# Performance work log

Hardware: AMD Instinct MI355X
Metric: run time of the kernel (lower is better)

## Reference

```python
import jax, jax.numpy as jnp
import numpy as np

NEG_INF = -9e15
ALPHA = 0.2  # LeakyReLU negative slope used by GraphAttentionLayer


def gat_layer(h, adj, W, a, concat):
    # h: [N, din], W: [din, dout], a: [2*dout, 1]
    Wh = h @ W                              # [N, dout]
    dout = W.shape[1]
    f1 = Wh @ a[:dout]                      # [N, 1]
    f2 = Wh @ a[dout:]                      # [N, 1]
    e = jax.nn.leaky_relu(f1 + f2.T, negative_slope=ALPHA)   # [N, N]
    att = jax.nn.softmax(jnp.where(adj > 0, e, NEG_INF), axis=1)
    hp = att @ Wh                           # [N, dout]
    out = jax.nn.elu(hp) if concat else hp
    return out, att


def setup_inputs() -> dict:
    key = jax.random.key(0)
    ks = jax.random.split(key, 6)
    N, d_in, d_hid, d_out = 8192, 256, 128, 64
    features = jax.random.normal(ks[0], (N, d_in), dtype=jnp.float32)
    adj = (jax.random.uniform(ks[1], (N, N)) < 0.01).astype(jnp.float32)
    s = 0.1
    W1 = jax.random.normal(ks[2], (d_in, d_hid), dtype=jnp.float32) * s
    a1 = jax.random.normal(ks[3], (2 * d_hid, 1), dtype=jnp.float32) * s
    W2 = jax.random.normal(ks[4], (d_hid, d_out), dtype=jnp.float32) * s
    a2 = jax.random.normal(ks[5], (2 * d_out, 1), dtype=jnp.float32) * s
    return {"features": features, "adj": adj, "W1": W1, "a1": a1, "W2": W2, "a2": a2}


def reference(features, adj, W1, a1, W2, a2):
    h1, attention = gat_layer(features, adj, W1, a1, concat=True)   # gat1 (elu)
    h2, _ = gat_layer(h1, adj, W2, a2, concat=False)                 # gat2
    row_mask = (adj.sum(axis=1) > 0).astype(h2.dtype)[:, None]       # [N, 1]
    genenet_res = jax.nn.sigmoid(h2 @ h2.T) * row_mask               # inner-product decoder
    return h2, genenet_res, attention
```

## Files before the change

kernel.cpp:

```cpp
#include <hip/hip_runtime.h>
#include <cstdint>
#include <cstddef>

#define NN 8192
#define DIN 256
#define DHID 128
#define DOUT 64
#define MAXDEG 256

using short8  = __attribute__((ext_vector_type(8))) short;
using floatx4 = __attribute__((ext_vector_type(4))) float;

__device__ inline unsigned short f2bf(float x) {
  union { float f; unsigned u; } c; c.f = x;
  unsigned r = (c.u + 0x7FFFu + ((c.u >> 16) & 1u)) >> 16;
  return (unsigned short)r;
}

__global__ __launch_bounds__(256) void k_gemm1(const float* __restrict__ feat,
                                               const float* __restrict__ W1,
                                               float* __restrict__ Wh1) {
  __shared__ float Ws[64 * DHID];
  __shared__ float Fs[32][65];
  const int tid = threadIdx.x;
  const int cx = tid & 31;
  const int ry = tid >> 5;
  const int r0 = blockIdx.x * 32;
  float acc[4][4] = {};
  for (int kc = 0; kc < DIN; kc += 64) {
    const float4* src = (const float4*)(W1 + (size_t)kc * DHID);
    float4* dst = (float4*)Ws;
    #pragma unroll
    for (int i = 0; i < 8; ++i) dst[i * 256 + tid] = src[i * 256 + tid];
    #pragma unroll
    for (int i = 0; i < 2; ++i) {
      int idx = i * 256 + tid;
      int row = idx >> 4, kq = idx & 15;
      float4 v = *(const float4*)(feat + (size_t)(r0 + row) * DIN + kc + kq * 4);
      Fs[row][kq * 4 + 0] = v.x; Fs[row][kq * 4 + 1] = v.y;
      Fs[row][kq * 4 + 2] = v.z; Fs[row][kq * 4 + 3] = v.w;
    }
    __syncthreads();
    #pragma unroll 4
    for (int k = 0; k < 64; ++k) {
      float4 w = *(const float4*)(Ws + k * DHID + cx * 4);
      #pragma unroll
      for (int r = 0; r < 4; ++r) {
        float f = Fs[ry * 4 + r][k];
        acc[r][0] += f * w.x; acc[r][1] += f * w.y;
        acc[r][2] += f * w.z; acc[r][3] += f * w.w;
      }
    }
    __syncthreads();
  }
  #pragma unroll
  for (int r = 0; r < 4; ++r) {
    float4 o = make_float4(acc[r][0], acc[r][1], acc[r][2], acc[r][3]);
    *(float4*)(Wh1 + (size_t)(r0 + ry * 4 + r) * DHID + cx * 4) = o;
  }
}

__global__ __launch_bounds__(256) void k_gemm2(const float* __restrict__ h1,
                                               const float* __restrict__ W2,
                                               float* __restrict__ Wh2) {
  __shared__ float Ws[64 * DOUT];
  __shared__ float Fs[32][65];
  const int tid = threadIdx.x;
  const int cx = tid & 15;
  const int ry = tid >> 4;
  const int r0 = blockIdx.x * 32;
  float acc[2][4] = {};
  for (int kc = 0; kc < DHID; kc += 64) {
    const float4* src = (const float4*)(W2 + (size_t)kc * DOUT);
    float4* dst = (float4*)Ws;
    #pragma unroll
    for (int i = 0; i < 4; ++i) dst[i * 256 + tid] = src[i * 256 + tid];
    #pragma unroll
    for (int i = 0; i < 2; ++i) {
      int idx = i * 256 + tid;
      int row = idx >> 4, kq = idx & 15;
      float4 v = *(const float4*)(h1 + (size_t)(r0 + row) * DHID + kc + kq * 4);
      Fs[row][kq * 4 + 0] = v.x; Fs[row][kq * 4 + 1] = v.y;
      Fs[row][kq * 4 + 2] = v.z; Fs[row][kq * 4 + 3] = v.w;
    }
    __syncthreads();
    #pragma unroll 4
    for (int k = 0; k < 64; ++k) {
      float4 w = *(const float4*)(Ws + k * DOUT + cx * 4);
      #pragma unroll
      for (int r = 0; r < 2; ++r) {
        float f = Fs[ry * 2 + r][k];
        acc[r][0] += f * w.x; acc[r][1] += f * w.y;
        acc[r][2] += f * w.z; acc[r][3] += f * w.w;
      }
    }
    __syncthreads();
  }
  #pragma unroll
  for (int r = 0; r < 2; ++r) {
    float4 o = make_float4(acc[r][0], acc[r][1], acc[r][2], acc[r][3]);
    *(float4*)(Wh2 + (size_t)(r0 + ry * 2 + r) * DOUT + cx * 4) = o;
  }
}

__global__ __launch_bounds__(256) void k_fvec1(const float* __restrict__ Wh1,
                                               const float* __restrict__ a1,
                                               float* __restrict__ f1, float* __restrict__ f2) {
  int wv = threadIdx.x >> 6, lane = threadIdx.x & 63;
  int row = blockIdx.x * 4 + wv;
  float2 x = *(const float2*)(Wh1 + (size_t)row * DHID + lane * 2);
  float2 u = *(const float2*)(a1 + lane * 2);
  float2 v = *(const float2*)(a1 + DHID + lane * 2);
  float s1 = x.x * u.x + x.y * u.y;
  float s2 = x.x * v.x + x.y * v.y;
  #pragma unroll
  for (int off = 32; off; off >>= 1) { s1 += __shfl_down(s1, off); s2 += __shfl_down(s2, off); }
  if (lane == 0) { f1[row] = s1; f2[row] = s2; }
}

__global__ __launch_bounds__(256) void k_fvec2(const float* __restrict__ Wh2,
                                               const float* __restrict__ a2,
                                               float* __restrict__ f1, float* __restrict__ f2) {
  int wv = threadIdx.x >> 6, lane = threadIdx.x & 63;
  int row = blockIdx.x * 4 + wv;
  float x = Wh2[(size_t)row * DOUT + lane];
  float s1 = x * a2[lane];
  float s2 = x * a2[DOUT + lane];
  #pragma unroll
  for (int off = 32; off; off >>= 1) { s1 += __shfl_down(s1, off); s2 += __shfl_down(s2, off); }
  if (lane == 0) { f1[row] = s1; f2[row] = s2; }
}

__global__ __launch_bounds__(256) void k_att1(const float* __restrict__ adj,
                                              const float* __restrict__ f1v,
                                              const float* __restrict__ f2v,
                                              const float* __restrict__ Wh1,
                                              float* __restrict__ att_out,
                                              float* __restrict__ h1,
                                              int* __restrict__ csr,
                                              int* __restrict__ degree) {
  __shared__ int   scols[4][MAXDEG];
  __shared__ float sval[4][MAXDEG];
  __shared__ int   cnt[4];
  const int tid = threadIdx.x;
  const int wid = tid >> 6, lane = tid & 63;
  const int row = blockIdx.x * 4 + wid;
  if (lane == 0) cnt[wid] = 0;
  __syncthreads();
  const float4* arow = (const float4*)(adj + (size_t)row * NN);
  #pragma unroll 4
  for (int it = 0; it < 32; ++it) {
    float4 v = arow[it * 64 + lane];
    int base = (it * 64 + lane) * 4;
    if (v.x > 0.0f) { int s = atomicAdd(&cnt[wid], 1); if (s < MAXDEG) scols[wid][s] = base; }
    if (v.y > 0.0f) { int s = atomicAdd(&cnt[wid], 1); if (s < MAXDEG) scols[wid][s] = base + 1; }
    if (v.z > 0.0f) { int s = atomicAdd(&cnt[wid], 1); if (s < MAXDEG) scols[wid][s] = base + 2; }
    if (v.w > 0.0f) { int s = atomicAdd(&cnt[wid], 1); if (s < MAXDEG) scols[wid][s] = base + 3; }
  }
  __syncthreads();
  const int deg = min(cnt[wid], MAXDEG);
  if (lane == 0) degree[row] = deg;
  if (deg == 0) {
    float4 fv = make_float4(1.0f / NN, 1.0f / NN, 1.0f / NN, 1.0f / NN);
    float4* orow = (float4*)(att_out + (size_t)row * NN);
    #pragma unroll 8
    for (int it = 0; it < 32; ++it) orow[it * 64 + lane] = fv;
  }
  for (int t = lane; t < deg; t += 64) csr[(size_t)row * MAXDEG + t] = scols[wid][t];
  const float f1r = f1v[row];
  float e[4]; int cols[4];
  float m = -3.0e38f;
  #pragma unroll
  for (int j = 0; j < 4; ++j) {
    int t = lane + j * 64;
    cols[j] = 0; e[j] = -3.0e38f;
    if (t < deg) {
      int c = scols[wid][t]; cols[j] = c;
      float x = f1r + f2v[c];
      e[j] = x > 0.0f ? x : 0.2f * x;
    }
    m = fmaxf(m, e[j]);
  }
  #pragma unroll
  for (int off = 32; off; off >>= 1) m = fmaxf(m, __shfl_xor(m, off));
  float ex[4]; float s = 0.0f;
  #pragma unroll
  for (int j = 0; j < 4; ++j) {
    ex[j] = __expf(e[j] - m);
    if (lane + j * 64 >= deg) ex[j] = 0.0f;
    s += ex[j];
  }
  #pragma unroll
  for (int off = 32; off; off >>= 1) s += __shfl_xor(s, off);
  const float inv = 1.0f / s;
  #pragma unroll
  for (int j = 0; j < 4; ++j) {
    int t = lane + j * 64;
    if (t < deg) {
      sval[wid][t] = ex[j] * inv;
      att_out[(size_t)row * NN + cols[j]] = ex[j] * inv;
    }
  }
  __syncthreads();
  float2 acc = make_float2(0.0f, 0.0f);
  if (deg > 0) {
    #pragma unroll 4
    for (int t = 0; t < deg; ++t) {
      float sv = sval[wid][t];
      float2 w = *(const float2*)(Wh1 + (size_t)scols[wid][t] * DHID + lane * 2);
      acc.x += sv * w.x; acc.y += sv * w.y;
    }
  } else {
    for (int r = 0; r < NN; ++r) {
      float2 w = *(const float2*)(Wh1 + (size_t)r * DHID + lane * 2);
      acc.x += w.x; acc.y += w.y;
    }
    acc.x *= (1.0f / (float)NN); acc.y *= (1.0f / (float)NN);
  }
  float hx = acc.x > 0.0f ? acc.x : (__expf(acc.x) - 1.0f);
  float hy = acc.y > 0.0f ? acc.y : (__expf(acc.y) - 1.0f);
  *(float2*)(h1 + (size_t)row * DHID + lane * 2) = make_float2(hx, hy);
}

__global__ __launch_bounds__(256) void k_att2(const int* __restrict__ csr,
                                              const int* __restrict__ degree,
                                              const float* __restrict__ f1v,
                                              const float* __restrict__ f2v,
                                              const float* __restrict__ Wh2,
                                              float* __restrict__ h2) {
  __shared__ int   scols[4][MAXDEG];
  __shared__ float sval[4][MAXDEG];
  const int tid = threadIdx.x;
  const int wid = tid >> 6, lane = tid & 63;
  const int row = blockIdx.x * 4 + wid;
  const int deg = degree[row];
  const float f1r = f1v[row];
  float e[4]; int cols[4];
  float m = -3.0e38f;
  #pragma unroll
  for (int j = 0; j < 4; ++j) {
    int t = lane + j * 64;
    cols[j] = 0; e[j] = -3.0e38f;
    if (t < deg) {
      int c = csr[(size_t)row * MAXDEG + t];
      cols[j] = c; scols[wid][t] = c;
      float x = f1r + f2v[c];
      e[j] = x > 0.0f ? x : 0.2f * x;
    }
    m = fmaxf(m, e[j]);
  }
  #pragma unroll
  for (int off = 32; off; off >>= 1) m = fmaxf(m, __shfl_xor(m, off));
  float ex[4]; float s = 0.0f;
  #pragma unroll
  for (int j = 0; j < 4; ++j) {
    ex[j] = __expf(e[j] - m);
    if (lane + j * 64 >= deg) ex[j] = 0.0f;
    s += ex[j];
  }
  #pragma unroll
  for (int off = 32; off; off >>= 1) s += __shfl_xor(s, off);
  const float inv = 1.0f / s;
  #pragma unroll
  for (int j = 0; j < 4; ++j) { int t = lane + j * 64; if (t < deg) sval[wid][t] = ex[j] * inv; }
  __syncthreads();
  float acc = 0.0f;
  if (deg > 0) {
    #pragma unroll 4
    for (int t = 0; t < deg; ++t)
      acc += sval[wid][t] * Wh2[(size_t)scols[wid][t] * DOUT + lane];
  } else {
    for (int r = 0; r < NN; ++r) acc += Wh2[(size_t)r * DOUT + lane];
    acc *= (1.0f / (float)NN);
  }
  h2[(size_t)row * DOUT + lane] = acc;
}

__global__ __launch_bounds__(256) void k_genenet(const float* __restrict__ h2,
                                                 const int* __restrict__ degree,
                                                 float* __restrict__ out) {
  __shared__ __align__(16) unsigned short AB[2 * 128 * 64];
  __shared__ float dmask[128];
  unsigned short* As = AB;
  unsigned short* Bs = AB + 128 * 64;
  const int tid = threadIdx.x;
  const int R0 = blockIdx.x * 128, C0 = blockIdx.y * 128;
  #pragma unroll
  for (int it = 0; it < 8; ++it) {
    int idx = it * 256 + tid;
    int r = idx >> 4, kq = idx & 15;
    int c = kq >> 1, hf = kq & 1;
    int off = r * 64 + (((c + r) & 7) << 3) + (hf << 2);
    float4 va = *(const float4*)(h2 + (size_t)(R0 + r) * DOUT + kq * 4);
    float4 vb = *(const float4*)(h2 + (size_t)(C0 + r) * DOUT + kq * 4);
    ushort4 ba = make_ushort4(f2bf(va.x), f2bf(va.y), f2bf(va.z), f2bf(va.w));
    ushort4 bb = make_ushort4(f2bf(vb.x), f2bf(vb.y), f2bf(vb.z), f2bf(vb.w));
    *(ushort4*)&As[off] = ba;
    *(ushort4*)&Bs[off] = bb;
  }
  if (tid < 128) dmask[tid] = (degree[R0 + tid] > 0) ? 1.0f : 0.0f;
  __syncthreads();
  const int wave = tid >> 6, lane = tid & 63;
  const int wr = wave >> 1, wc = wave & 1;
  const int lr = lane & 15, quad = lane >> 4;
  short8 a[4][2], b[4][2];
  #pragma unroll
  for (int mi = 0; mi < 4; ++mi) {
    int r = wr * 64 + mi * 16 + lr;
    #pragma unroll
    for (int j = 0; j < 2; ++j) {
      int c = quad + 4 * j;
      a[mi][j] = *(const short8*)(const void*)&As[r * 64 + (((c + r) & 7) << 3)];
    }
  }
  #pragma unroll
  for (int ni = 0; ni < 4; ++ni) {
    int r = wc * 64 + ni * 16 + lr;
    #pragma unroll
    for (int j = 0; j < 2; ++j) {
      int c = quad + 4 * j;
      b[ni][j] = *(const short8*)(const void*)&Bs[r * 64 + (((c + r) & 7) << 3)];
    }
  }
  floatx4 acc[4][4] = {};
  #pragma unroll
  for (int mi = 0; mi < 4; ++mi)
    #pragma unroll
    for (int ni = 0; ni < 4; ++ni) {
      acc[mi][ni] = __builtin_amdgcn_mfma_f32_16x16x32_bf16(a[mi][0], b[ni][0], acc[mi][ni], 0, 0, 0);
      acc[mi][ni] = __builtin_amdgcn_mfma_f32_16x16x32_bf16(a[mi][1], b[ni][1], acc[mi][ni], 0, 0, 0);
    }
  __syncthreads();
  float* stage = (float*)AB;
  #pragma unroll
  for (int half = 0; half < 2; ++half) {
    if (wr == half) {
      #pragma unroll
      for (int mi = 0; mi < 4; ++mi)
        #pragma unroll
        for (int reg = 0; reg < 4; ++reg) {
          int lrow = mi * 16 + quad * 4 + reg;
          #pragma unroll
          for (int ni = 0; ni < 4; ++ni)
            stage[lrow * 128 + wc * 64 + ni * 16 + lr] = acc[mi][ni][reg];
        }
    }
    __syncthreads();
    #pragma unroll
    for (int it = 0; it < 8; ++it) {
      int idx = it * 256 + tid;
      int r = idx >> 5, c4 = idx & 31;
      float4 x = *(const float4*)&stage[r * 128 + c4 * 4];
      float msk = dmask[half * 64 + r];
      floatx4 o;
      o[0] = msk * __builtin_amdgcn_rcpf(1.0f + __expf(-x.x));
      o[1] = msk * __builtin_amdgcn_rcpf(1.0f + __expf(-x.y));
      o[2] = msk * __builtin_amdgcn_rcpf(1.0f + __expf(-x.z));
      o[3] = msk * __builtin_amdgcn_rcpf(1.0f + __expf(-x.w));
      __builtin_nontemporal_store(o, (floatx4*)(out + (size_t)(R0 + half * 64 + r) * NN + C0 + c4 * 4));
    }
    if (half == 0) __syncthreads();
  }
}

extern "C" void kernel_launch(void* const* d_in, const int* in_sizes, int n_in,
                              void* d_out, int out_size, void* d_ws, size_t ws_size,
                              hipStream_t stream) {
  const float* feat = (const float*)d_in[0];
  const float* adj  = (const float*)d_in[1];
  const float* W1   = (const float*)d_in[2];
  const float* a1   = (const float*)d_in[3];
  const float* W2   = (const float*)d_in[4];
  const float* a2   = (const float*)d_in[5];
  float* out = (float*)d_out;
  float* h2_out  = out;
  float* gen_out = out + (size_t)NN * DOUT;
  float* att_out = gen_out + (size_t)NN * NN;
  int*   csr  = (int*)gen_out;
  float* Wh1  = gen_out + 2097152;
  float* h1   = gen_out + 3145728;
  float* Wh2  = gen_out + 4194304;
  float* f1_1 = gen_out + 4718592;
  float* f2_1 = f1_1 + NN;
  float* f1_2 = f2_1 + NN;
  float* f2_2 = f1_2 + NN;
  int* degree = (int*)d_ws;

  (void)hipMemsetAsync((void*)att_out, 0, (size_t)NN * NN * sizeof(float), stream);

  k_gemm1  <<<dim3(NN / 32), dim3(256), 0, stream>>>(feat, W1, Wh1);
  k_fvec1  <<<dim3(NN / 4),  dim3(256), 0, stream>>>(Wh1, a1, f1_1, f2_1);
  k_att1   <<<dim3(NN / 4),  dim3(256), 0, stream>>>(adj, f1_1, f2_1, Wh1, att_out, h1, csr, degree);
  k_gemm2  <<<dim3(NN / 32), dim3(256), 0, stream>>>(h1, W2, Wh2);
  k_fvec2  <<<dim3(NN / 4),  dim3(256), 0, stream>>>(Wh2, a2, f1_2, f2_2);
  k_att2   <<<dim3(NN / 4),  dim3(256), 0, stream>>>(csr, degree, f1_2, f2_2, Wh2, h2_out);
  k_genenet<<<dim3(64, 64),  dim3(256), 0, stream>>>(h2_out, degree, gen_out);
}
```

Baseline: 798.4 us.

## Fuse attention-vector dots into GEMMs and write dense attention rows directly

The f1/f2 projections are now computed in the GEMM epilogues with a lane-group shuffle reduction, which removes the two fvec kernels and a reread of Wh. The 256MB memset of the attention matrix is also removed. k_att1 builds a per-row bitmap of the adjacency in shared memory and then writes every attention row as dense nontemporal float4 stores, recomputing each nonzero value in place. Entries for columns beyond the first MAXDEG neighbors are now written as nonzero, while before they stayed zero, so results could differ for rows that hit the cap.

Result: no change. 787.2 us (-1.4%).

```diff
diff --git a/kernel.cpp b/kernel.cpp
--- a/kernel.cpp
+++ b/kernel.cpp
@@ -19,7 +19,10 @@
 
 __global__ __launch_bounds__(256) void k_gemm1(const float* __restrict__ feat,
                                                const float* __restrict__ W1,
-                                               float* __restrict__ Wh1) {
+                                               const float* __restrict__ a1,
+                                               float* __restrict__ Wh1,
+                                               float* __restrict__ f1,
+                                               float* __restrict__ f2) {
   __shared__ float Ws[64 * DHID];
   __shared__ float Fs[32][65];
   const int tid = threadIdx.x;
@@ -53,16 +56,26 @@
     }
     __syncthreads();
   }
+  const float4 u = *(const float4*)(a1 + cx * 4);
+  const float4 v = *(const float4*)(a1 + DHID + cx * 4);
   #pragma unroll
   for (int r = 0; r < 4; ++r) {
     float4 o = make_float4(acc[r][0], acc[r][1], acc[r][2], acc[r][3]);
     *(float4*)(Wh1 + (size_t)(r0 + ry * 4 + r) * DHID + cx * 4) = o;
+    float s1 = acc[r][0] * u.x + acc[r][1] * u.y + acc[r][2] * u.z + acc[r][3] * u.w;
+    float s2 = acc[r][0] * v.x + acc[r][1] * v.y + acc[r][2] * v.z + acc[r][3] * v.w;
+    #pragma unroll
+    for (int off = 16; off; off >>= 1) { s1 += __shfl_xor(s1, off); s2 += __shfl_xor(s2, off); }
+    if (cx == 0) { f1[r0 + ry * 4 + r] = s1; f2[r0 + ry * 4 + r] = s2; }
   }
 }
 
 __global__ __launch_bounds__(256) void k_gemm2(const float* __restrict__ h1,
                                                const float* __restrict__ W2,
-                                               float* __restrict__ Wh2) {
+                                               const float* __restrict__ a2,
+                                               float* __restrict__ Wh2,
+                                               float* __restrict__ f1,
+                                               float* __restrict__ f2) {
   __shared__ float Ws[64 * DOUT];
   __shared__ float Fs[32][65];
   const int tid = threadIdx.x;
@@ -96,39 +109,18 @@
     }
     __syncthreads();
   }
+  const float4 u = *(const float4*)(a2 + cx * 4);
+  const float4 v = *(const float4*)(a2 + DOUT + cx * 4);
   #pragma unroll
   for (int r = 0; r < 2; ++r) {
     float4 o = make_float4(acc[r][0], acc[r][1], acc[r][2], acc[r][3]);
     *(float4*)(Wh2 + (size_t)(r0 + ry * 2 + r) * DOUT + cx * 4) = o;
-  }
-}
-
-__global__ __launch_bounds__(256) void k_fvec1(const float* __restrict__ Wh1,
-                                               const float* __restrict__ a1,
-                                               float* __restrict__ f1, float* __restrict__ f2) {
-  int wv = threadIdx.x >> 6, lane = threadIdx.x & 63;
-  int row = blockIdx.x * 4 + wv;
-  float2 x = *(const float2*)(Wh1 + (size_t)row * DHID + lane * 2);
-  float2 u = *(const float2*)(a1 + lane * 2);
-  float2 v = *(const float2*)(a1 + DHID + lane * 2);
-  float s1 = x.x * u.x + x.y * u.y;
-  float s2 = x.x * v.x + x.y * v.y;
-  #pragma unroll
-  for (int off = 32; off; off >>= 1) { s1 += __shfl_down(s1, off); s2 += __shfl_down(s2, off); }
-  if (lane == 0) { f1[row] = s1; f2[row] = s2; }
-}
-
-__global__ __launch_bounds__(256) void k_fvec2(const float* __restrict__ Wh2,
-                                               const float* __restrict__ a2,
-                                               float* __restrict__ f1, float* __restrict__ f2) {
-  int wv = threadIdx.x >> 6, lane = threadIdx.x & 63;
-  int row = blockIdx.x * 4 + wv;
-  float x = Wh2[(size_t)row * DOUT + lane];
-  float s1 = x * a2[lane];
-  float s2 = x * a2[DOUT + lane];
-  #pragma unroll
-  for (int off = 32; off; off >>= 1) { s1 += __shfl_down(s1, off); s2 += __shfl_down(s2, off); }
-  if (lane == 0) { f1[row] = s1; f2[row] = s2; }
+    float s1 = acc[r][0] * u.x + acc[r][1] * u.y + acc[r][2] * u.z + acc[r][3] * u.w;
+    float s2 = acc[r][0] * v.x + acc[r][1] * v.y + acc[r][2] * v.z + acc[r][3] * v.w;
+    #pragma unroll
+    for (int off = 8; off; off >>= 1) { s1 += __shfl_xor(s1, off); s2 += __shfl_xor(s2, off); }
+    if (cx == 0) { f1[r0 + ry * 2 + r] = s1; f2[r0 + ry * 2 + r] = s2; }
+  }
 }
 
 __global__ __launch_bounds__(256) void k_att1(const float* __restrict__ adj,
@@ -139,9 +131,10 @@
                                               float* __restrict__ h1,
                                               int* __restrict__ csr,
                                               int* __restrict__ degree) {
-  __shared__ int   scols[4][MAXDEG];
-  __shared__ float sval[4][MAXDEG];
-  __shared__ int   cnt[4];
+  __shared__ int      scols[4][MAXDEG];
+  __shared__ float    sval[4][MAXDEG];
+  __shared__ unsigned bitmap[4][NN / 32];
+  __shared__ int      cnt[4];
   const int tid = threadIdx.x;
   const int wid = tid >> 6, lane = tid & 63;
   const int row = blockIdx.x * 4 + wid;
@@ -152,30 +145,31 @@
   for (int it = 0; it < 32; ++it) {
     float4 v = arow[it * 64 + lane];
     int base = (it * 64 + lane) * 4;
+    unsigned nib = (v.x > 0.0f ? 1u : 0u) | (v.y > 0.0f ? 2u : 0u)
+                 | (v.z > 0.0f ? 4u : 0u) | (v.w > 0.0f ? 8u : 0u);
     if (v.x > 0.0f) { int s = atomicAdd(&cnt[wid], 1); if (s < MAXDEG) scols[wid][s] = base; }
     if (v.y > 0.0f) { int s = atomicAdd(&cnt[wid], 1); if (s < MAXDEG) scols[wid][s] = base + 1; }
     if (v.z > 0.0f) { int s = atomicAdd(&cnt[wid], 1); if (s < MAXDEG) scols[wid][s] = base + 2; }
     if (v.w > 0.0f) { int s = atomicAdd(&cnt[wid], 1); if (s < MAXDEG) scols[wid][s] = base + 3; }
+    unsigned wbits = nib << ((lane & 7) * 4);
+    wbits |= __shfl_xor(wbits, 1);
+    wbits |= __shfl_xor(wbits, 2);
+    wbits |= __shfl_xor(wbits, 4);
+    if ((lane & 7) == 0) bitmap[wid][it * 8 + (lane >> 3)] = wbits;
   }
   __syncthreads();
   const int deg = min(cnt[wid], MAXDEG);
   if (lane == 0) degree[row] = deg;
-  if (deg == 0) {
-    float4 fv = make_float4(1.0f / NN, 1.0f / NN, 1.0f / NN, 1.0f / NN);
-    float4* orow = (float4*)(att_out + (size_t)row * NN);
-    #pragma unroll 8
-    for (int it = 0; it < 32; ++it) orow[it * 64 + lane] = fv;
-  }
   for (int t = lane; t < deg; t += 64) csr[(size_t)row * MAXDEG + t] = scols[wid][t];
   const float f1r = f1v[row];
-  float e[4]; int cols[4];
+  float e[4];
   float m = -3.0e38f;
   #pragma unroll
   for (int j = 0; j < 4; ++j) {
     int t = lane + j * 64;
-    cols[j] = 0; e[j] = -3.0e38f;
+    e[j] = -3.0e38f;
     if (t < deg) {
-      int c = scols[wid][t]; cols[j] = c;
+      int c = scols[wid][t];
       float x = f1r + f2v[c];
       e[j] = x > 0.0f ? x : 0.2f * x;
     }
@@ -194,12 +188,25 @@
   for (int off = 32; off; off >>= 1) s += __shfl_xor(s, off);
   const float inv = 1.0f / s;
   #pragma unroll
-  for (int j = 0; j < 4; ++j) {
-    int t = lane + j * 64;
-    if (t < deg) {
-      sval[wid][t] = ex[j] * inv;
-      att_out[(size_t)row * NN + cols[j]] = ex[j] * inv;
-    }
+  for (int j = 0; j < 4; ++j) { int t = lane + j * 64; if (t < deg) sval[wid][t] = ex[j] * inv; }
+  const float fillv = (deg == 0) ? (1.0f / (float)NN) : 0.0f;
+  floatx4* orow = (floatx4*)(att_out + (size_t)row * NN);
+  for (int it = 0; it < 32; ++it) {
+    unsigned wbits = bitmap[wid][it * 8 + (lane >> 3)];
+    unsigned nib = (wbits >> ((lane & 7) * 4)) & 0xFu;
+    int base = (it * 64 + lane) * 4;
+    floatx4 o = {fillv, fillv, fillv, fillv};
+    if (nib) {
+      #pragma unroll
+      for (int k = 0; k < 4; ++k) {
+        if (nib & (1u << k)) {
+          float x = f1r + f2v[base + k];
+          float ee = x > 0.0f ? x : 0.2f * x;
+          o[k] = __expf(ee - m) * inv;
+        }
+      }
+    }
+    __builtin_nontemporal_store(o, orow + it * 64 + lane);
   }
   __syncthreads();
   float2 acc = make_float2(0.0f, 0.0f);
@@ -235,15 +242,15 @@
   const int row = blockIdx.x * 4 + wid;
   const int deg = degree[row];
   const float f1r = f1v[row];
-  float e[4]; int cols[4];
+  float e[4];
   float m = -3.0e38f;
   #pragma unroll
   for (int j = 0; j < 4; ++j) {
     int t = lane + j * 64;
-    cols[j] = 0; e[j] = -3.0e38f;
+    e[j] = -3.0e38f;
     if (t < deg) {
       int c = csr[(size_t)row * MAXDEG + t];
-      cols[j] = c; scols[wid][t] = c;
+      scols[wid][t] = c;
       float x = f1r + f2v[c];
       e[j] = x > 0.0f ? x : 0.2f * x;
     }
@@ -386,13 +393,9 @@
   float* f2_2 = f1_2 + NN;
   int* degree = (int*)d_ws;
 
-  (void)hipMemsetAsync((void*)att_out, 0, (size_t)NN * NN * sizeof(float), stream);
-
-  k_gemm1  <<<dim3(NN / 32), dim3(256), 0, stream>>>(feat, W1, Wh1);
-  k_fvec1  <<<dim3(NN / 4),  dim3(256), 0, stream>>>(Wh1, a1, f1_1, f2_1);
+  k_gemm1  <<<dim3(NN / 32), dim3(256), 0, stream>>>(feat, W1, a1, Wh1, f1_1, f2_1);
   k_att1   <<<dim3(NN / 4),  dim3(256), 0, stream>>>(adj, f1_1, f2_1, Wh1, att_out, h1, csr, degree);
-  k_gemm2  <<<dim3(NN / 32), dim3(256), 0, stream>>>(h1, W2, Wh2);
-  k_fvec2  <<<dim3(NN / 4),  dim3(256), 0, stream>>>(Wh2, a2, f1_2, f2_2);
+  k_gemm2  <<<dim3(NN / 32), dim3(256), 0, stream>>>(h1, W2, a2, Wh2, f1_2, f2_2);
   k_att2   <<<dim3(NN / 4),  dim3(256), 0, stream>>>(csr, degree, f1_2, f2_2, Wh2, h2_out);
   k_genenet<<<dim3(64, 64),  dim3(256), 0, stream>>>(h2_out, degree, gen_out);
 }
```
